# Optimization experiments

Measured on AMD Instinct MI355X. Metric: run time of the kernel, lower is better.

## Reference

```python
import jax, jax.numpy as jnp
import numpy as np

D_MODEL = 768
N_HEADS = 12
D_HEAD = D_MODEL // N_HEADS


def setup_inputs() -> dict:
    key = jax.random.key(0)
    k1, k2, k3 = jax.random.split(key, 3)
    x = jax.random.normal(k1, (2, 4096, D_MODEL), dtype=jnp.float32)
    # nn.Linear weights stored as (out_features, in_features); y = x @ W.T
    w_qkv = jax.random.normal(k2, (3 * D_MODEL, D_MODEL), dtype=jnp.float32) * 0.02
    w_out = jax.random.normal(k3, (D_MODEL, D_MODEL), dtype=jnp.float32) * 0.02
    return {"x": x, "w_qkv": w_qkv, "w_out": w_out}


def reference(x, w_qkv, w_out):
    B, T, d_model = x.shape
    scale = jnp.float32(np.sqrt(D_HEAD))
    qkv = jnp.einsum('btd,ed->bte', x, w_qkv)            # (B,T,3*d_model)
    q, k, v = jnp.split(qkv, 3, axis=-1)
    # (B,T,H,Dh) -> (B,H,T,Dh)
    q = q.reshape(B, T, N_HEADS, D_HEAD).transpose(0, 2, 1, 3)
    k = k.reshape(B, T, N_HEADS, D_HEAD).transpose(0, 2, 1, 3)
    v = v.reshape(B, T, N_HEADS, D_HEAD).transpose(0, 2, 1, 3)
    scores = jnp.einsum('bhqd,bhkd->bhqk', q, k) / scale  # (B,H,T,T)
    causal = jnp.tril(jnp.ones((T, T), dtype=bool))       # True = keep
    scores = jnp.where(causal[None, None], scores, jnp.float32(-jnp.inf))
    attn = jax.nn.softmax(scores, axis=-1)
    out = jnp.einsum('bhqk,bhkd->bhqd', attn, v)          # (B,H,T,Dh)
    out = out.transpose(0, 2, 1, 3).reshape(B, T, d_model)
    out = jnp.einsum('btd,ed->bte', out, w_out)
    return out
```

## Files before the change

### kernel.cpp

```cpp
#include <hip/hip_runtime.h>
#include <hip/hip_bf16.h>

typedef __attribute__((ext_vector_type(8))) short bf16x8;
typedef __attribute__((ext_vector_type(4))) float f32x4;
typedef __attribute__((ext_vector_type(16))) float f32x16;

#define D_MODEL 768
#define N_HEADS 12
#define D_HEAD  64
#define SEQ     4096
#define BATCH   2
#define MROWS   (BATCH * SEQ)
#define QKV_N   (3 * D_MODEL)
#define NBH     (BATCH * N_HEADS)
#define SCL     0.18033688011112042f

#define SWZ(row) ((((row) & 7) ^ (((row) >> 3) & 3)))

#define GLOAD_LDS16(gsrc, ldst) \
    __builtin_amdgcn_global_load_lds( \
        (const __attribute__((address_space(1))) int*)(gsrc), \
        (__attribute__((address_space(3))) int*)(ldst), 16, 0, 0)

__global__ __launch_bounds__(256) void cvt_all(const float* __restrict__ x,  unsigned short* __restrict__ xb,  int nx4,
                                               const float* __restrict__ wq, unsigned short* __restrict__ wqb, int nq4,
                                               const float* __restrict__ wo, unsigned short* __restrict__ wob, int no4) {
    int i = blockIdx.x * blockDim.x + threadIdx.x;
    const float* in;
    unsigned short* out;
    int idx;
    if (i < nx4)                   { in = x;  out = xb;  idx = i; }
    else if (i < nx4 + nq4)        { in = wq; out = wqb; idx = i - nx4; }
    else if (i < nx4 + nq4 + no4)  { in = wo; out = wob; idx = i - nx4 - nq4; }
    else return;
    const float4 v = *(const float4*)(in + (size_t)idx * 4);
    ushort4 o;
    o.x = __bfloat16_as_ushort(__float2bfloat16(v.x));
    o.y = __bfloat16_as_ushort(__float2bfloat16(v.y));
    o.z = __bfloat16_as_ushort(__float2bfloat16(v.z));
    o.w = __bfloat16_as_ushort(__float2bfloat16(v.w));
    *(ushort4*)(out + (size_t)idx * 4) = o;
}

#define BM 128
#define BN 128
#define BK 64

template <bool OUT_F32, bool WRITE_VT>
__global__ __launch_bounds__(256) void gemm_bt(const short* __restrict__ A,
                                               const short* __restrict__ B,
                                               float* __restrict__ Cf,
                                               unsigned short* __restrict__ Cb,
                                               unsigned short* __restrict__ vt,
                                               int M, int N, int K) {
    __shared__ __align__(16) short As[BM][BK];
    __shared__ __align__(16) short Bs[BN][BK];

    const int tid  = threadIdx.x;
    const int m0   = blockIdx.y * BM;
    const int n0   = blockIdx.x * BN;
    const int w    = tid >> 6;
    const int lane = tid & 63;
    const int wr   = w >> 1, wc = w & 1;
    const int lr   = lane & 15, lhi = lane >> 4;

    int srow[4], sga[4];
#pragma unroll
    for (int s = 0; s < 4; s++) {
        int idx = (w * 4 + s) * 64 + lane;
        srow[s] = idx >> 3;
        sga[s]  = (idx & 7) ^ (srow[s] & 7);
    }

    f32x4 acc[4][4];
#pragma unroll
    for (int i = 0; i < 4; i++)
#pragma unroll
        for (int j = 0; j < 4; j++)
#pragma unroll
            for (int e = 0; e < 4; e++) acc[i][j][e] = 0.0f;

    for (int k0 = 0; k0 < K; k0 += BK) {
#pragma unroll
        for (int s = 0; s < 4; s++) {
            GLOAD_LDS16(&A[(size_t)(m0 + srow[s]) * K + k0 + sga[s] * 8],
                        (short*)As + (w * 4 + s) * 512);
            GLOAD_LDS16(&B[(size_t)(n0 + srow[s]) * K + k0 + sga[s] * 8],
                        (short*)Bs + (w * 4 + s) * 512);
        }
        __syncthreads();
#pragma unroll
        for (int c = 0; c < 2; ++c) {
            bf16x8 af[4], bfr[4];
#pragma unroll
            for (int mi = 0; mi < 4; mi++) {
                int row = wr * 64 + mi * 16 + lr;
                af[mi] = *(const bf16x8*)&As[row][((c * 4 + lhi) ^ (lr & 7)) * 8];
            }
#pragma unroll
            for (int ni = 0; ni < 4; ni++) {
                int row = wc * 64 + ni * 16 + lr;
                bfr[ni] = *(const bf16x8*)&Bs[row][((c * 4 + lhi) ^ (lr & 7)) * 8];
            }
#pragma unroll
            for (int mi = 0; mi < 4; mi++)
#pragma unroll
                for (int ni = 0; ni < 4; ni++)
                    acc[mi][ni] = __builtin_amdgcn_mfma_f32_16x16x32_bf16(af[mi], bfr[ni], acc[mi][ni], 0, 0, 0);
        }
        __syncthreads();
    }

#pragma unroll
    for (int mi = 0; mi < 4; mi++)
#pragma unroll
        for (int ni = 0; ni < 4; ni++) {
            const int col  = n0 + wc * 64 + ni * 16 + lr;
            const int row0 = m0 + wr * 64 + mi * 16 + lhi * 4;
            if (WRITE_VT && col >= 2 * D_MODEL) {
                const int hd = col - 2 * D_MODEL;
                const int h2 = hd >> 6, d = hd & 63;
                const int b2 = row0 >> 12, t = row0 & (SEQ - 1);
                ushort4 p;
                p.x = __bfloat16_as_ushort(__float2bfloat16(acc[mi][ni][0]));
                p.y = __bfloat16_as_ushort(__float2bfloat16(acc[mi][ni][1]));
                p.z = __bfloat16_as_ushort(__float2bfloat16(acc[mi][ni][2]));
                p.w = __bfloat16_as_ushort(__float2bfloat16(acc[mi][ni][3]));
                *(ushort4*)&vt[((size_t)(b2 * N_HEADS + h2) * 64 + d) * SEQ + t] = p;
            } else {
                const float qs = (WRITE_VT && col < D_MODEL) ? SCL : 1.0f;
#pragma unroll
                for (int r = 0; r < 4; r++) {
                    float v = acc[mi][ni][r] * qs;
                    if (OUT_F32)
                        Cf[(size_t)(row0 + r) * N + col] = v;
                    else
                        Cb[(size_t)(row0 + r) * N + col] = __bfloat16_as_ushort(__float2bfloat16(v));
                }
            }
        }
}

__device__ __forceinline__ unsigned cvt_pk_bf16(float lo, float hi) {
    unsigned r;
    asm("v_cvt_pk_bf16_f32 %0, %1, %2" : "=v"(r) : "v"(lo), "v"(hi));
    return r;
}

__global__ __launch_bounds__(256) void attn_fwd(const short* __restrict__ qkv,
                                                const short* __restrict__ vt,
                                                unsigned short* __restrict__ pO,
                                                float* __restrict__ pL) {
    __shared__ __align__(16) short Ks[2][64][64];
    __shared__ __align__(16) short Vs[2][64][64];

    const int tid  = threadIdx.x;
    const int w    = tid >> 6;
    const int lane = tid & 63;
    const int l31  = lane & 31;
    const int hi   = lane >> 5;
    const int swzk = SWZ(l31);
    const int flat = blockIdx.x;
    const int i    = 31 - flat / (2 * NBH);
    const int rem  = flat % (2 * NBH);
    const int half = rem / NBH;
    const int bh   = rem % NBH;
    const int b    = bh / N_HEADS, h = bh % N_HEADS;
    const size_t rowbase = (size_t)b * SEQ;
    const int q0   = i * 128;
    const int qw   = q0 + w * 32;
    const int qg   = qw + l31;
    const int srow = tid >> 3, sg = tid & 7;

    const int ts = half ? (i + 1) : 0;
    const int te = half ? (2 * i + 2) : (i + 1);

    bf16x8 ones;
#pragma unroll
    for (int j = 0; j < 8; j++) ones[j] = (short)0x3F80;

    bf16x8 qf[4];
    {
        const short* qp = &qkv[(rowbase + qg) * QKV_N + h * D_HEAD + hi * 8];
#pragma unroll
        for (int c = 0; c < 4; c++) qf[c] = *(const bf16x8*)&qp[c * 16];
    }

    f32x16 oacc[2], lacc;
#pragma unroll
    for (int e = 0; e < 16; e++) { oacc[0][e] = 0.0f; oacc[1][e] = 0.0f; lacc[e] = 0.0f; }

    bf16x8 kp[2], vp[2];
#pragma unroll
    for (int s = 0; s < 2; s++) {
        int row = srow + 32 * s;
        kp[s] = *(const bf16x8*)&qkv[(rowbase + ts * 64 + row) * QKV_N + D_MODEL + h * D_HEAD + sg * 8];
        vp[s] = *(const bf16x8*)&vt[((size_t)bh * 64 + row) * SEQ + ts * 64 + sg * 8];
    }

    for (int jt = ts; jt < te; jt++) {
        const int j0  = jt * 64;
        const int cur = jt & 1;
#pragma unroll
        for (int s = 0; s < 2; s++) {
            int row = srow + 32 * s;
            int dst = (sg ^ SWZ(row)) * 8;
            *(bf16x8*)&Ks[cur][row][dst] = kp[s];
            *(bf16x8*)&Vs[cur][row][dst] = vp[s];
        }
        {
            int jn = (jt + 1 < te) ? j0 + 64 : ts * 64;
#pragma unroll
            for (int s = 0; s < 2; s++) {
                int row = srow + 32 * s;
                kp[s] = *(const bf16x8*)&qkv[(rowbase + jn + row) * QKV_N + D_MODEL + h * D_HEAD + sg * 8];
                vp[s] = *(const bf16x8*)&vt[((size_t)bh * 64 + row) * SEQ + jn + sg * 8];
            }
        }
        __syncthreads();

        if (j0 > qw + 31) continue;
        const bool skip1 = (j0 >= qw);

        f32x16 sa0, sa1;
#pragma unroll
        for (int e = 0; e < 16; e++) { sa0[e] = 0.0f; sa1[e] = 0.0f; }
        __builtin_amdgcn_s_setprio(1);
#pragma unroll
        for (int c = 0; c < 4; c++) {
            bf16x8 kf0 = *(const bf16x8*)&Ks[cur][l31][((2 * c + hi) ^ swzk) * 8];
            sa0 = __builtin_amdgcn_mfma_f32_32x32x16_bf16(kf0, qf[c], sa0, 0, 0, 0);
        }
        if (!skip1) {
#pragma unroll
            for (int c = 0; c < 4; c++) {
                bf16x8 kf1 = *(const bf16x8*)&Ks[cur][32 + l31][((2 * c + hi) ^ swzk) * 8];
                sa1 = __builtin_amdgcn_mfma_f32_32x32x16_bf16(kf1, qf[c], sa1, 0, 0, 0);
            }
        }
        __builtin_amdgcn_s_setprio(0);

        if (j0 + 63 > qw) {
#pragma unroll
            for (int g = 0; g < 4; g++)
#pragma unroll
                for (int r = 0; r < 4; r++) {
                    int kloc = r + 8 * g + 4 * hi;
                    if (j0 + kloc > qg) sa0[g * 4 + r] = -INFINITY;
                    if (!skip1 && j0 + 32 + kloc > qg) sa1[g * 4 + r] = -INFINITY;
                }
        }

#pragma unroll
        for (int e = 0; e < 16; e++) sa0[e] = __builtin_amdgcn_exp2f(sa0[e]);
        if (!skip1) {
#pragma unroll
            for (int e = 0; e < 16; e++) sa1[e] = __builtin_amdgcn_exp2f(sa1[e]);
        }

        bf16x8 pa0, pa1, pa2, pa3;
        {
            unsigned X[4], U[4];
#pragma unroll
            for (int g = 0; g < 4; g++) {
                X[g] = cvt_pk_bf16(sa0[4 * g + 0], sa0[4 * g + 1]);
                U[g] = cvt_pk_bf16(sa0[4 * g + 2], sa0[4 * g + 3]);
            }
            asm("v_permlane32_swap_b32 %0, %1" : "+v"(X[0]), "+v"(X[1]));
            asm("v_permlane32_swap_b32 %0, %1" : "+v"(U[0]), "+v"(U[1]));
            asm("v_permlane32_swap_b32 %0, %1" : "+v"(X[2]), "+v"(X[3]));
            asm("v_permlane32_swap_b32 %0, %1" : "+v"(U[2]), "+v"(U[3]));
            union { unsigned u[4]; bf16x8 v; } q0_, q1_;
            q0_.u[0] = X[0]; q0_.u[1] = U[0]; q0_.u[2] = X[1]; q0_.u[3] = U[1];
            q1_.u[0] = X[2]; q1_.u[1] = U[2]; q1_.u[2] = X[3]; q1_.u[3] = U[3];
            pa0 = q0_.v; pa1 = q1_.v;
        }
        if (!skip1) {
            unsigned X[4], U[4];
#pragma unroll
            for (int g = 0; g < 4; g++) {
                X[g] = cvt_pk_bf16(sa1[4 * g + 0], sa1[4 * g + 1]);
                U[g] = cvt_pk_bf16(sa1[4 * g + 2], sa1[4 * g + 3]);
            }
            asm("v_permlane32_swap_b32 %0, %1" : "+v"(X[0]), "+v"(X[1]));
            asm("v_permlane32_swap_b32 %0, %1" : "+v"(U[0]), "+v"(U[1]));
            asm("v_permlane32_swap_b32 %0, %1" : "+v"(X[2]), "+v"(X[3]));
            asm("v_permlane32_swap_b32 %0, %1" : "+v"(U[2]), "+v"(U[3]));
            union { unsigned u[4]; bf16x8 v; } q0_, q1_;
            q0_.u[0] = X[0]; q0_.u[1] = U[0]; q0_.u[2] = X[1]; q0_.u[3] = U[1];
            q1_.u[0] = X[2]; q1_.u[1] = U[2]; q1_.u[2] = X[3]; q1_.u[3] = U[3];
            pa2 = q0_.v; pa3 = q1_.v;
        } else {
            pa2 = pa0; pa3 = pa1;
        }

        __builtin_amdgcn_s_setprio(1);
        lacc = __builtin_amdgcn_mfma_f32_32x32x16_bf16(pa0, ones, lacc, 0, 0, 0);
        lacc = __builtin_amdgcn_mfma_f32_32x32x16_bf16(pa1, ones, lacc, 0, 0, 0);
        if (!skip1) {
            lacc = __builtin_amdgcn_mfma_f32_32x32x16_bf16(pa2, ones, lacc, 0, 0, 0);
            lacc = __builtin_amdgcn_mfma_f32_32x32x16_bf16(pa3, ones, lacc, 0, 0, 0);
        }
#pragma unroll
        for (int nd = 0; nd < 2; nd++) {
            const int vrow = nd * 32 + l31;
            const int vswz = SWZ(vrow);
            bf16x8 vb0 = *(const bf16x8*)&Vs[cur][vrow][((0 + hi) ^ vswz) * 8];
            oacc[nd] = __builtin_amdgcn_mfma_f32_32x32x16_bf16(pa0, vb0, oacc[nd], 0, 0, 0);
            bf16x8 vb1 = *(const bf16x8*)&Vs[cur][vrow][((2 + hi) ^ vswz) * 8];
            oacc[nd] = __builtin_amdgcn_mfma_f32_32x32x16_bf16(pa1, vb1, oacc[nd], 0, 0, 0);
            if (!skip1) {
                bf16x8 vb2 = *(const bf16x8*)&Vs[cur][vrow][((4 + hi) ^ vswz) * 8];
                oacc[nd] = __builtin_amdgcn_mfma_f32_32x32x16_bf16(pa2, vb2, oacc[nd], 0, 0, 0);
                bf16x8 vb3 = *(const bf16x8*)&Vs[cur][vrow][((6 + hi) ^ vswz) * 8];
                oacc[nd] = __builtin_amdgcn_mfma_f32_32x32x16_bf16(pa3, vb3, oacc[nd], 0, 0, 0);
            }
        }
        __builtin_amdgcn_s_setprio(0);
    }

#pragma unroll
    for (int g = 0; g < 4; g++)
#pragma unroll
        for (int r = 0; r < 4; r++) {
            const int qrow = qw + r + 8 * g + 4 * hi;
            const size_t rh = ((size_t)half * MROWS + rowbase + qrow) * N_HEADS + h;
            if (l31 == 0) pL[rh] = lacc[g * 4 + r];
#pragma unroll
            for (int nd = 0; nd < 2; nd++)
                pO[rh * D_HEAD + nd * 32 + l31] =
                    __bfloat16_as_ushort(__float2bfloat16(oacc[nd][g * 4 + r]));
        }
}

__global__ __launch_bounds__(256) void attn_combine(const unsigned short* __restrict__ pO,
                                                    const float* __restrict__ pL,
                                                    unsigned short* __restrict__ out) {
    const int t  = blockIdx.x * 256 + threadIdx.x;
    const int dg = t & 7;
    const int rh = t >> 3;
    const int h  = rh % N_HEADS;
    const int row = rh / N_HEADS;
    const size_t rh0 = (size_t)row * N_HEADS + h;
    const size_t rh1 = ((size_t)MROWS + row) * N_HEADS + h;
    const float inv = 1.0f / (pL[rh0] + pL[rh1]);
    bf16x8 a = *(const bf16x8*)&pO[rh0 * D_HEAD + dg * 8];
    bf16x8 c = *(const bf16x8*)&pO[rh1 * D_HEAD + dg * 8];
    unsigned short o[8];
#pragma unroll
    for (int j = 0; j < 8; j++) {
        float va = __bfloat162float(__ushort_as_bfloat16((unsigned short)a[j]));
        float vc = __bfloat162float(__ushort_as_bfloat16((unsigned short)c[j]));
        o[j] = __bfloat16_as_ushort(__float2bfloat16((va + vc) * inv));
    }
    *(bf16x8*)&out[(size_t)row * D_MODEL + h * D_HEAD + dg * 8] = *(bf16x8*)o;
}

extern "C" void kernel_launch(void* const* d_in, const int* in_sizes, int n_in,
                              void* d_out, int out_size, void* d_ws, size_t ws_size,
                              hipStream_t stream) {
    const float* x     = (const float*)d_in[0];
    const float* w_qkv = (const float*)d_in[1];
    const float* w_out = (const float*)d_in[2];
    float* outp        = (float*)d_out;

    char* ws = (char*)d_ws;
    size_t off = 0;
    auto alloc = [&](size_t bytes) -> void* {
        void* p = ws + off;
        off = (off + bytes + 255) & ~(size_t)255;
        return p;
    };
    unsigned short* xb    = (unsigned short*)alloc((size_t)MROWS * D_MODEL * 2);
    unsigned short* wqkvb = (unsigned short*)alloc((size_t)QKV_N * D_MODEL * 2);
    unsigned short* woutb = (unsigned short*)alloc((size_t)D_MODEL * D_MODEL * 2);
    unsigned short* qkvb  = (unsigned short*)alloc((size_t)MROWS * QKV_N * 2);
    unsigned short* vtb   = (unsigned short*)alloc((size_t)NBH * D_HEAD * SEQ * 2);
    unsigned short* pOb   = (unsigned short*)alloc((size_t)2 * MROWS * N_HEADS * D_HEAD * 2);
    float*          pLb   = (float*)alloc((size_t)2 * MROWS * N_HEADS * 4);

    {
        const int nx4 = MROWS * D_MODEL / 4;
        const int nq4 = QKV_N * D_MODEL / 4;
        const int no4 = D_MODEL * D_MODEL / 4;
        const int tot = nx4 + nq4 + no4;
        cvt_all<<<(tot + 255) / 256, 256, 0, stream>>>(x, xb, nx4, w_qkv, wqkvb, nq4, w_out, woutb, no4);
    }

    gemm_bt<false, true><<<dim3(QKV_N / BN, MROWS / BM), 256, 0, stream>>>(
        (const short*)xb, (const short*)wqkvb, nullptr, qkvb, vtb, MROWS, QKV_N, D_MODEL);

    attn_fwd<<<dim3(32 * 2 * NBH), 256, 0, stream>>>(
        (const short*)qkvb, (const short*)vtb, pOb, pLb);

    attn_combine<<<dim3(MROWS * N_HEADS * 8 / 256), 256, 0, stream>>>(pOb, pLb, xb);

    gemm_bt<true, false><<<dim3(D_MODEL / BN, MROWS / BM), 256, 0, stream>>>(
        (const short*)xb, (const short*)woutb, outp, nullptr, nullptr, MROWS, D_MODEL, D_MODEL);
}
```

Baseline: 189.6 us.

## Double attention query tile to 256 rows with 512-thread blocks

The attention kernel now runs 8 waves per block over 256 query rows instead of 4 waves over 128, so each K/V tile staged in LDS serves twice as many queries. Each thread now loads one K row and one V row per tile instead of two, and the prefetch uses incrementing pointers. The grid is halved. This cuts global K/V traffic per query and the per-thread load work, but gives coarser work units, fewer blocks for load balance across the causal split, and more masked work per block near the diagonal.

```diff
diff --git a/kernel.cpp b/kernel.cpp
--- a/kernel.cpp
+++ b/kernel.cpp
@@ -147,7 +147,7 @@
     return r;
 }
 
-__global__ __launch_bounds__(256) void attn_fwd(const short* __restrict__ qkv,
+__global__ __launch_bounds__(512) void attn_fwd(const short* __restrict__ qkv,
                                                 const short* __restrict__ vt,
                                                 unsigned short* __restrict__ pO,
                                                 float* __restrict__ pL) {
@@ -161,19 +161,19 @@
     const int hi   = lane >> 5;
     const int swzk = SWZ(l31);
     const int flat = blockIdx.x;
-    const int i    = 31 - flat / (2 * NBH);
+    const int i    = 15 - flat / (2 * NBH);
     const int rem  = flat % (2 * NBH);
     const int half = rem / NBH;
     const int bh   = rem % NBH;
     const int b    = bh / N_HEADS, h = bh % N_HEADS;
     const size_t rowbase = (size_t)b * SEQ;
-    const int q0   = i * 128;
+    const int q0   = i * 256;
     const int qw   = q0 + w * 32;
     const int qg   = qw + l31;
     const int srow = tid >> 3, sg = tid & 7;
 
-    const int ts = half ? (i + 1) : 0;
-    const int te = half ? (2 * i + 2) : (i + 1);
+    const int ts = half ? (2 * i + 2) : 0;
+    const int te = half ? (4 * i + 4) : (2 * i + 2);
 
     bf16x8 ones;
 #pragma unroll
@@ -190,33 +190,21 @@
 #pragma unroll
     for (int e = 0; e < 16; e++) { oacc[0][e] = 0.0f; oacc[1][e] = 0.0f; lacc[e] = 0.0f; }
 
-    bf16x8 kp[2], vp[2];
-#pragma unroll
-    for (int s = 0; s < 2; s++) {
-        int row = srow + 32 * s;
-        kp[s] = *(const bf16x8*)&qkv[(rowbase + ts * 64 + row) * QKV_N + D_MODEL + h * D_HEAD + sg * 8];
-        vp[s] = *(const bf16x8*)&vt[((size_t)bh * 64 + row) * SEQ + ts * 64 + sg * 8];
-    }
+    const short* kptr = &qkv[(rowbase + ts * 64 + srow) * QKV_N + D_MODEL + h * D_HEAD + sg * 8];
+    const short* vptr = &vt[((size_t)bh * 64 + srow) * SEQ + ts * 64 + sg * 8];
+    bf16x8 kp = *(const bf16x8*)kptr;
+    bf16x8 vp = *(const bf16x8*)vptr;
+
+    const int dst = (sg ^ SWZ(srow)) * 8;
 
     for (int jt = ts; jt < te; jt++) {
         const int j0  = jt * 64;
         const int cur = jt & 1;
-#pragma unroll
-        for (int s = 0; s < 2; s++) {
-            int row = srow + 32 * s;
-            int dst = (sg ^ SWZ(row)) * 8;
-            *(bf16x8*)&Ks[cur][row][dst] = kp[s];
-            *(bf16x8*)&Vs[cur][row][dst] = vp[s];
-        }
-        {
-            int jn = (jt + 1 < te) ? j0 + 64 : ts * 64;
-#pragma unroll
-            for (int s = 0; s < 2; s++) {
-                int row = srow + 32 * s;
-                kp[s] = *(const bf16x8*)&qkv[(rowbase + jn + row) * QKV_N + D_MODEL + h * D_HEAD + sg * 8];
-                vp[s] = *(const bf16x8*)&vt[((size_t)bh * 64 + row) * SEQ + jn + sg * 8];
-            }
-        }
+        *(bf16x8*)&Ks[cur][srow][dst] = kp;
+        *(bf16x8*)&Vs[cur][srow][dst] = vp;
+        if (jt + 1 < te) { kptr += 64 * QKV_N; vptr += 64; }
+        kp = *(const bf16x8*)kptr;
+        vp = *(const bf16x8*)vptr;
         __syncthreads();
 
         if (j0 > qw + 31) continue;
@@ -390,7 +378,7 @@
     gemm_bt<false, true><<<dim3(QKV_N / BN, MROWS / BM), 256, 0, stream>>>(
         (const short*)xb, (const short*)wqkvb, nullptr, qkvb, vtb, MROWS, QKV_N, D_MODEL);
 
-    attn_fwd<<<dim3(32 * 2 * NBH), 256, 0, stream>>>(
+    attn_fwd<<<dim3(16 * 2 * NBH), 512, 0, stream>>>(
         (const short*)qkvb, (const short*)vtb, pOb, pLb);
 
     attn_combine<<<dim3(MROWS * N_HEADS * 8 / 256), 256, 0, stream>>>(pOb, pLb, xb);
```

Measured after the change: 161.5 us. -14.8%, faster.
